# Kernel tuning notes

Hardware: AMD Instinct MI355X
Metric: run time of the kernel (lower is better)

## Reference

```python
import jax, jax.numpy as jnp
import numpy as np
from jax import lax

B, S, E, H, NB, F, NQ, NC = 256, 196, 256, 8, 4, 1024, 8, 10


def _ln(x, g, b, eps=1e-5):
    m = x.mean(-1, keepdims=True)
    v = ((x - m) ** 2).mean(-1, keepdims=True)
    return (x - m) / jnp.sqrt(v + eps) * g + b


def _pe(s, e):
    pos = jnp.arange(s, dtype=jnp.float32)[:, None]
    div = jnp.exp(jnp.arange(0, e, 2, dtype=jnp.float32) * (-np.log(10000.0) / e))
    ang = pos * div  # [S, E/2]
    # even indices sin, odd indices cos -> interleave
    return jnp.stack([jnp.sin(ang), jnp.cos(ang)], axis=-1).reshape(s, e)


def setup_inputs() -> dict:
    key = jax.random.key(0)
    ks = jax.random.split(key, 16)
    r = lambda i, shape, s=0.05: jax.random.normal(ks[i], shape, dtype=jnp.float32) * s
    return {
        'x': jax.random.normal(ks[0], (B, 4, 28, 28), dtype=jnp.float32),
        'qfilter_w': r(1, (4, 1, 2, 2), 0.3), 'qfilter_b': jnp.zeros(4, jnp.float32),
        'pw_w': r(2, (4, 4, 1, 1), 0.3), 'pw_b': jnp.zeros(4, jnp.float32),
        'embed_w': r(3, (E, 4), 0.3), 'embed_b': jnp.zeros(E, jnp.float32),
        'in_proj_w': r(4, (NB, 3 * E, E)), 'in_proj_b': jnp.zeros((NB, 3 * E), jnp.float32),
        'out_w': r(5, (NB, E, E)), 'out_b': jnp.zeros((NB, E), jnp.float32),
        'theta': r(6, (NB, NQ), 1.0),
        'l1_w': r(7, (NB, F, NQ), 0.3), 'l1_b': jnp.zeros((NB, F), jnp.float32),
        'l2_w': r(8, (NB, E, F)), 'l2_b': jnp.zeros((NB, E), jnp.float32),
        'ln1_g': jnp.ones((NB, E), jnp.float32), 'ln1_b': jnp.zeros((NB, E), jnp.float32),
        'ln2_g': jnp.ones((NB, E), jnp.float32), 'ln2_b': jnp.zeros((NB, E), jnp.float32),
        'cls_w': r(9, (NC, E)), 'cls_b': jnp.zeros(NC, jnp.float32),
    }


def reference(x, qfilter_w, qfilter_b, pw_w, pw_b, embed_w, embed_b,
              in_proj_w, in_proj_b, out_w, out_b, theta,
              l1_w, l1_b, l2_w, l2_b, ln1_g, ln1_b, ln2_g, ln2_b, cls_w, cls_b):
    dn = ('NCHW', 'OIHW', 'NCHW')
    # depthwise 2x2 stride-2 quanvolution filter (groups=4)
    feat = lax.conv_general_dilated(x, qfilter_w, (2, 2), 'VALID',
                                    dimension_numbers=dn, feature_group_count=4)
    feat = feat + qfilter_b[None, :, None, None]
    # 1x1 pointwise conv
    feat = lax.conv_general_dilated(feat, pw_w, (1, 1), 'VALID', dimension_numbers=dn)
    feat = feat + pw_b[None, :, None, None]
    b = x.shape[0]
    feat = feat.reshape(b, S, 4)  # channel-major view, faithful to torch .view
    h = feat @ embed_w.T + embed_b
    h = h + _pe(S, E)[None]
    hd = E // H
    scale = 1.0 / np.sqrt(hd)
    for i in range(NB):
        # multi-head self-attention
        qkv = h @ in_proj_w[i].T + in_proj_b[i]
        q, k, v = jnp.split(qkv, 3, axis=-1)
        q = q.reshape(b, S, H, hd).transpose(0, 2, 1, 3)
        k = k.reshape(b, S, H, hd).transpose(0, 2, 1, 3)
        v = v.reshape(b, S, H, hd).transpose(0, 2, 1, 3)
        scores = jnp.einsum('bhsd,bhtd->bhst', q, k) * scale
        a = jax.nn.softmax(scores, axis=-1)
        o = jnp.einsum('bhst,bhtd->bhsd', a, v).transpose(0, 2, 1, 3).reshape(b, S, E)
        o = o @ out_w[i].T + out_b[i]
        h = _ln(h + o, ln1_g[i], ln1_b[i])
        # quantum FFN: RX(x_j) then RY(theta_j) on |0>, <Z> = cos(x_j)cos(theta_j)
        qm = jnp.cos(h[..., :NQ]) * jnp.cos(theta[i])  # [b, S, NQ]
        f = jax.nn.relu(qm @ l1_w[i].T + l1_b[i]) @ l2_w[i].T + l2_b[i]
        h = _ln(h + f, ln2_g[i], ln2_b[i])
    pooled = h.mean(axis=1)
    return pooled @ cls_w.T + cls_b
```

## Files before the change

### kernel.cpp

```cpp
#include <hip/hip_runtime.h>
#include <math.h>

#define BATCH 256
#define SEQ   196
#define EMB   256
#define HEADS 8
#define HDIM  32
#define NBLK  4
#define FDIM  1024
#define NQB   8
#define NCLS  10
#define MROWS (BATCH*SEQ)

typedef __attribute__((ext_vector_type(8))) short  short8;
typedef __attribute__((ext_vector_type(4))) float  floatx4;

__device__ __forceinline__ unsigned short f2b(float f) {
    unsigned u = __builtin_bit_cast(unsigned, f);
    u += 0x7fffu + ((u >> 16) & 1u);
    return (unsigned short)(u >> 16);
}
__device__ __forceinline__ float b2f(unsigned short u) {
    return __builtin_bit_cast(float, ((unsigned)u) << 16);
}

__device__ __forceinline__ void gl_lds16(const void* g, void* l) {
    __builtin_amdgcn_global_load_lds(
        (const __attribute__((address_space(1))) unsigned int*)g,
        (__attribute__((address_space(3))) unsigned int*)l, 16, 0, 0);
}

#define QSCALE (0.17677669529663687f * 1.4426950408889634f)

__global__ void pe_kernel(float* __restrict__ pe) {
    int s = blockIdx.x, e = threadIdx.x;
    int j2 = (e >> 1) * 2;
    float dv  = expf(-(float)j2 * (logf(10000.0f) / (float)EMB));
    float ang = (float)s * dv;
    pe[s * EMB + e] = (e & 1) ? cosf(ang) : sinf(ang);
}

__global__ __launch_bounds__(256) void cvt_kernel(
    const float* __restrict__ src, unsigned short* __restrict__ dst, int n)
{
    int i = (blockIdx.x * 256 + threadIdx.x) * 4;
    if (i < n) {
        float4 v = *(const float4*)(src + i);
        ushort4 o;
        o.x = f2b(v.x); o.y = f2b(v.y); o.z = f2b(v.z); o.w = f2b(v.w);
        *(ushort4*)(dst + i) = o;
    }
}

__global__ __launch_bounds__(256) void l1t_kernel(
    const float* __restrict__ src, float* __restrict__ dst)
{
    int idx = blockIdx.x * 256 + threadIdx.x;
    int i = idx >> 13, rem = idx & 8191;
    int q = rem & 7, f = rem >> 3;
    dst[((size_t)i * NQB + q) * FDIM + f] = src[idx];
}

__global__ __launch_bounds__(256) void feat_kernel(
    const float* __restrict__ x,  const float* __restrict__ qw,
    const float* __restrict__ qb, const float* __restrict__ pw,
    const float* __restrict__ pb, float* __restrict__ feat)
{
    int idx = blockIdx.x * 256 + threadIdx.x;
    int bs = idx >> 2, c = idx & 3;
    int b  = bs / SEQ, s = bs % SEQ;
    int co = s / 49;
    int p  = (s % 49) * 4 + c;
    int hh = p / 14, ww = p % 14;

    float dw[4];
#pragma unroll
    for (int ci = 0; ci < 4; ++ci) {
        const float* xp = x + (((size_t)b * 4 + ci) * 28 + hh * 2) * 28 + ww * 2;
        dw[ci] = qb[ci] + xp[0]  * qw[ci * 4 + 0] + xp[1]  * qw[ci * 4 + 1]
                        + xp[28] * qw[ci * 4 + 2] + xp[29] * qw[ci * 4 + 3];
    }
    feat[idx] = pb[co] + pw[co * 4 + 0] * dw[0] + pw[co * 4 + 1] * dw[1]
                       + pw[co * 4 + 2] * dw[2] + pw[co * 4 + 3] * dw[3];
}

__global__ __launch_bounds__(256) void embed2_kernel(
    const float* __restrict__ feat, const float* __restrict__ ew,
    const float* __restrict__ eb,   const float* __restrict__ pe,
    unsigned short* __restrict__ hb)
{
    __shared__ float fL[32 * 4];
    int t = threadIdx.x;
    int base = blockIdx.x * 32;

    if (t < 128) fL[t] = feat[(size_t)base * 4 + t];
    __syncthreads();

    float4 w4  = *(const float4*)(ew + t * 4);
    float  ebv = eb[t];
    int s = base % SEQ;
#pragma unroll 4
    for (int tt = 0; tt < 32; ++tt) {
        float4 f = *(const float4*)&fL[tt * 4];
        float v = ebv + f.x * w4.x + f.y * w4.y + f.z * w4.z + f.w * w4.w
                + pe[s * EMB + t];
        hb[(size_t)(base + tt) * EMB + t] = f2b(v);
        if (++s == SEQ) s = 0;
    }
}

__global__ __launch_bounds__(512) void bgemm_kernel(
    const unsigned short* __restrict__ A, const unsigned short* __restrict__ W,
    const float* __restrict__ bias, unsigned short* __restrict__ Cb,
    int M, int N, int K, int qcols, float qscale)
{
    __shared__ unsigned short As[128 * 64];
    __shared__ unsigned short Bs[128 * 64];

    int t = threadIdx.x;
    int w = t >> 6, l = t & 63;
    int quad = l >> 4, lane16 = l & 15;
    int m0 = blockIdx.y * 128, n0 = blockIdx.x * 128;
    int mq = (w >> 2) * 64;
    int nq = (w & 3) * 32;

    int lr8  = l >> 3;
    int scol = ((l & 7) ^ lr8) * 8;
    int srow = w * 16 + lr8;
    const unsigned short* Abase = A + (size_t)(m0 + srow) * K + scol;
    const unsigned short* Wbase = W + (size_t)(n0 + srow) * K + scol;
    unsigned short* AsW = As + w * 16 * 64;
    unsigned short* BsW = Bs + w * 16 * 64;

    floatx4 acc[4][2];
#pragma unroll
    for (int i = 0; i < 4; ++i)
#pragma unroll
        for (int j = 0; j < 2; ++j) acc[i][j] = (floatx4){0.f, 0.f, 0.f, 0.f};

    int key = lane16 & 7;

    for (int k0 = 0; k0 < K; k0 += 64) {
        __syncthreads();
#pragma unroll
        for (int c = 0; c < 2; ++c) {
            gl_lds16(Abase + (size_t)c * 8 * K + k0, AsW + c * 512);
            gl_lds16(Wbase + (size_t)c * 8 * K + k0, BsW + c * 512);
        }
        __syncthreads();

#pragma unroll
        for (int kk = 0; kk < 2; ++kk) {
            int ch = ((kk * 4 + quad) ^ key) * 8;
            short8 af[4], bf[2];
#pragma unroll
            for (int i = 0; i < 4; ++i)
                af[i] = *(const short8*)&As[(mq + i * 16 + lane16) * 64 + ch];
#pragma unroll
            for (int j = 0; j < 2; ++j)
                bf[j] = *(const short8*)&Bs[(nq + j * 16 + lane16) * 64 + ch];
#pragma unroll
            for (int i = 0; i < 4; ++i)
#pragma unroll
                for (int j = 0; j < 2; ++j)
                    acc[i][j] = __builtin_amdgcn_mfma_f32_16x16x32_bf16(
                                    af[i], bf[j], acc[i][j], 0, 0, 0);
        }
    }

#pragma unroll
    for (int j = 0; j < 2; ++j) {
        int col = n0 + nq + j * 16 + lane16;
        float bb  = bias[col];
        float mul = (col < qcols) ? qscale : 1.0f;
#pragma unroll
        for (int i = 0; i < 4; ++i) {
#pragma unroll
            for (int r = 0; r < 4; ++r) {
                int row = m0 + mq + i * 16 + quad * 4 + r;
                Cb[(size_t)row * N + col] = f2b((acc[i][j][r] + bb) * mul);
            }
        }
    }
}

__global__ __launch_bounds__(512) void bgemm_ln_kernel(
    const unsigned short* __restrict__ A, const unsigned short* __restrict__ W,
    const float* __restrict__ bias, const float* __restrict__ g,
    const float* __restrict__ beta, const float* __restrict__ theta,
    const unsigned short* __restrict__ Rb, unsigned short* __restrict__ OutB,
    float* __restrict__ qm, int K)
{
    __shared__ unsigned short As[64 * 64];
    __shared__ unsigned short Bs[256 * 64];
    __shared__ float redS[64][4], redQ[64][4];
    __shared__ float mrow[64], irow[64];

    int t = threadIdx.x;
    int w = t >> 6, l = t & 63;
    int quad = l >> 4, lane16 = l & 15;
    int m0 = blockIdx.x * 64;

    int wq = w >> 2;
    int cg = w & 3;
    int nq = cg * 64;

    int lr8  = l >> 3;
    int lc8s = ((l & 7) ^ lr8) * 8;
    const unsigned short* Abase = A + (size_t)(m0 + w * 8 + lr8) * K + lc8s;
    const unsigned short* Wbase = W + (size_t)(w * 8 + lr8) * K + lc8s;
    unsigned short* AsW = As + w * 8 * 64;
    unsigned short* BsW = Bs + w * 8 * 64;

    floatx4 acc[2][4];
#pragma unroll
    for (int i = 0; i < 2; ++i)
#pragma unroll
        for (int j = 0; j < 4; ++j) acc[i][j] = (floatx4){0.f, 0.f, 0.f, 0.f};

    int key = lane16 & 7;

    for (int k0 = 0; k0 < K; k0 += 64) {
        __syncthreads();
        gl_lds16(Abase + k0, AsW);
#pragma unroll
        for (int c = 0; c < 4; ++c)
            gl_lds16(Wbase + (size_t)c * 64 * K + k0, BsW + c * 64 * 64);
        __syncthreads();

#pragma unroll
        for (int kk = 0; kk < 2; ++kk) {
            int ch = ((kk * 4 + quad) ^ key) * 8;
            short8 af[2], bf[4];
#pragma unroll
            for (int i = 0; i < 2; ++i)
                af[i] = *(const short8*)&As[(wq * 32 + i * 16 + lane16) * 64 + ch];
#pragma unroll
            for (int j = 0; j < 4; ++j)
                bf[j] = *(const short8*)&Bs[(nq + j * 16 + lane16) * 64 + ch];
#pragma unroll
            for (int i = 0; i < 2; ++i)
#pragma unroll
                for (int j = 0; j < 4; ++j)
                    acc[i][j] = __builtin_amdgcn_mfma_f32_16x16x32_bf16(
                                    af[i], bf[j], acc[i][j], 0, 0, 0);
        }
    }

    float bb[4];
#pragma unroll
    for (int j = 0; j < 4; ++j) bb[j] = bias[nq + j * 16 + lane16];

#pragma unroll
    for (int i = 0; i < 2; ++i) {
#pragma unroll
        for (int r = 0; r < 4; ++r) {
            int row = wq * 32 + i * 16 + quad * 4 + r;
            const unsigned short* rp = Rb + (size_t)(m0 + row) * EMB;
            float s1 = 0.f, s2 = 0.f;
#pragma unroll
            for (int j = 0; j < 4; ++j) {
                float v = acc[i][j][r] + bb[j] + b2f(rp[nq + j * 16 + lane16]);
                acc[i][j][r] = v;
                s1 += v;
                s2 += v * v;
            }
#pragma unroll
            for (int off = 8; off >= 1; off >>= 1) {
                s1 += __shfl_xor(s1, off);
                s2 += __shfl_xor(s2, off);
            }
            if (lane16 == 0) { redS[row][cg] = s1; redQ[row][cg] = s2; }
        }
    }
    __syncthreads();

    if (t < 64) {
        float s1 = redS[t][0] + redS[t][1] + redS[t][2] + redS[t][3];
        float s2 = redQ[t][0] + redQ[t][1] + redQ[t][2] + redQ[t][3];
        float mean = s1 * (1.0f / 256.0f);
        float var  = s2 * (1.0f / 256.0f) - mean * mean;
        mrow[t] = mean;
        irow[t] = rsqrtf(var + 1e-5f);
    }
    __syncthreads();

    float gv[4], bv[4];
#pragma unroll
    for (int j = 0; j < 4; ++j) {
        int col = nq + j * 16 + lane16;
        gv[j] = g[col];
        bv[j] = beta[col];
    }

#pragma unroll
    for (int i = 0; i < 2; ++i) {
#pragma unroll
        for (int r = 0; r < 4; ++r) {
            int row  = wq * 32 + i * 16 + quad * 4 + r;
            float mean = mrow[row], inv = irow[row];
            size_t base = (size_t)(m0 + row) * EMB;
#pragma unroll
            for (int j = 0; j < 4; ++j) {
                int col = nq + j * 16 + lane16;
                float y = (acc[i][j][r] - mean) * inv * gv[j] + bv[j];
                OutB[base + col] = f2b(y);
                if (qm && cg == 0 && j == 0 && lane16 < NQB)
                    qm[(size_t)(m0 + row) * NQB + lane16] =
                        __cosf(y) * __cosf(theta[lane16]);
            }
        }
    }
}

__global__ __launch_bounds__(256) void act_kernel(
    const float* __restrict__ qm, const float* __restrict__ l1wT,
    const float* __restrict__ l1b, unsigned short* __restrict__ act)
{
    __shared__ float qL[16 * NQB];
    int t  = threadIdx.x;
    int m0 = blockIdx.x * 16;

    if (t < 128) qL[t] = qm[(size_t)m0 * NQB + t];

    int f  = (t & 127) * 8;
    int r0 = (t >> 7) * 8;

    float4 wv0[8], wv1[8];
#pragma unroll
    for (int j = 0; j < 8; ++j) {
        wv0[j] = *(const float4*)(l1wT + (size_t)j * FDIM + f);
        wv1[j] = *(const float4*)(l1wT + (size_t)j * FDIM + f + 4);
    }
    float4 b0 = *(const float4*)(l1b + f);
    float4 b1 = *(const float4*)(l1b + f + 4);
    __syncthreads();

#pragma unroll
    for (int rr = 0; rr < 8; ++rr) {
        int row = r0 + rr;
        const float* q = &qL[row * NQB];
        float4 a0 = b0, a1 = b1;
#pragma unroll
        for (int j = 0; j < 8; ++j) {
            float qj = q[j];
            a0.x += qj * wv0[j].x; a0.y += qj * wv0[j].y;
            a0.z += qj * wv0[j].z; a0.w += qj * wv0[j].w;
            a1.x += qj * wv1[j].x; a1.y += qj * wv1[j].y;
            a1.z += qj * wv1[j].z; a1.w += qj * wv1[j].w;
        }
        unsigned short o[8];
        o[0] = f2b(fmaxf(a0.x, 0.f)); o[1] = f2b(fmaxf(a0.y, 0.f));
        o[2] = f2b(fmaxf(a0.z, 0.f)); o[3] = f2b(fmaxf(a0.w, 0.f));
        o[4] = f2b(fmaxf(a1.x, 0.f)); o[5] = f2b(fmaxf(a1.y, 0.f));
        o[6] = f2b(fmaxf(a1.z, 0.f)); o[7] = f2b(fmaxf(a1.w, 0.f));
        *(short8*)(act + (size_t)(m0 + row) * FDIM + f) = *(short8*)o;
    }
}

__global__ __launch_bounds__(256, 3) void attn_kernel(
    const unsigned short* __restrict__ qkv, unsigned short* __restrict__ ob)
{
    __shared__ unsigned short Vt[32 * 232];
    __shared__ unsigned short Ps[64 * 232];

    int t  = threadIdx.x;
    int bh = blockIdx.x;
    int b  = bh >> 3;
    int hh = bh & 7;
    const unsigned short* base = qkv + (size_t)b * SEQ * 768 + hh * HDIM;

    for (int idx = t; idx < SEQ * 8; idx += 256) {
        int s = idx >> 3, d4 = (idx & 7) * 4;
        ushort4 vv = *(const ushort4*)(base + (size_t)s * 768 + 512 + d4);
        Vt[(d4 + 0) * 232 + s] = vv.x;
        Vt[(d4 + 1) * 232 + s] = vv.y;
        Vt[(d4 + 2) * 232 + s] = vv.z;
        Vt[(d4 + 3) * 232 + s] = vv.w;
    }
    for (int idx = t; idx < 32 * 36; idx += 256) {
        int d = idx / 36, c = 196 + idx % 36;
        Vt[d * 232 + c] = 0;
    }
    for (int idx = t; idx < 64 * 24; idx += 256) {
        int r = idx / 24, c = 208 + idx % 24;
        Ps[r * 232 + c] = 0;
    }

    int w = t >> 6, l = t & 63;
    int quad = l >> 4, lane16 = l & 15;
    unsigned short* Pw = Ps + w * 16 * 232;

    short8 kf[13];
#pragma unroll
    for (int kt = 0; kt < 13; ++kt)
        kf[kt] = *(const short8*)(base + (size_t)(kt * 16 + lane16) * 768 + 256 + quad * 8);

    __syncthreads();

    for (int qt = w; qt < 13; qt += 4) {
        short8 af = *(const short8*)(base + (size_t)(qt * 16 + lane16) * 768 + quad * 8);

        floatx4 sc[13];
#pragma unroll
        for (int kt = 0; kt < 13; ++kt) {
            floatx4 z = {0.f, 0.f, 0.f, 0.f};
            sc[kt] = __builtin_amdgcn_mfma_f32_16x16x32_bf16(af, kf[kt], z, 0, 0, 0);
        }

        float lsum[4] = {0.f, 0.f, 0.f, 0.f};
#pragma unroll
        for (int kt = 0; kt < 13; ++kt) {
#pragma unroll
            for (int r = 0; r < 4; ++r) {
                float v = sc[kt][r];
                if (kt == 12 && lane16 >= 4) v = -1e30f;
                float p = exp2f(v);
                lsum[r] += p;
                Pw[(quad * 4 + r) * 232 + kt * 16 + lane16] = f2b(p);
            }
        }
#pragma unroll
        for (int off = 8; off >= 1; off >>= 1)
#pragma unroll
            for (int r = 0; r < 4; ++r)
                lsum[r] += __shfl_xor(lsum[r], off);

        floatx4 oacc[2] = {{0.f,0.f,0.f,0.f},{0.f,0.f,0.f,0.f}};
#pragma unroll
        for (int c = 0; c < 7; ++c) {
            short8 pa = *(const short8*)&Pw[lane16 * 232 + c * 32 + quad * 8];
#pragma unroll
            for (int nt = 0; nt < 2; ++nt) {
                short8 vb = *(const short8*)&Vt[(nt * 16 + lane16) * 232 + c * 32 + quad * 8];
                oacc[nt] = __builtin_amdgcn_mfma_f32_16x16x32_bf16(pa, vb, oacc[nt], 0, 0, 0);
            }
        }

#pragma unroll
        for (int r = 0; r < 4; ++r) {
            int srow = qt * 16 + quad * 4 + r;
            if (srow < SEQ) {
                float invl = 1.f / lsum[r];
                unsigned short* op = ob + ((size_t)b * SEQ + srow) * EMB + hh * HDIM;
                op[lane16]      = f2b(oacc[0][r] * invl);
                op[16 + lane16] = f2b(oacc[1][r] * invl);
            }
        }
    }
}

__global__ __launch_bounds__(256) void pool_cls_kernel(
    const unsigned short* __restrict__ hb, const float* __restrict__ cw,
    const float* __restrict__ cb, float* __restrict__ out)
{
    __shared__ float pooled[EMB];
    int b = blockIdx.x;
    int e = threadIdx.x;
    float s = 0.f;
    const unsigned short* hp = hb + (size_t)b * SEQ * EMB + e;
    for (int j = 0; j < SEQ; ++j) s += b2f(hp[(size_t)j * EMB]);
    pooled[e] = s * (1.0f / (float)SEQ);
    __syncthreads();
    if (e < NCLS) {
        float acc = cb[e];
        const float* wr = cw + e * EMB;
        for (int k = 0; k < EMB; ++k) acc += pooled[k] * wr[k];
        out[b * NCLS + e] = acc;
    }
}

extern "C" void kernel_launch(void* const* d_in, const int* in_sizes, int n_in,
                              void* d_out, int out_size, void* d_ws, size_t ws_size,
                              hipStream_t stream)
{
    const float* x         = (const float*)d_in[0];
    const float* qfilter_w = (const float*)d_in[1];
    const float* qfilter_b = (const float*)d_in[2];
    const float* pw_w      = (const float*)d_in[3];
    const float* pw_b      = (const float*)d_in[4];
    const float* embed_w   = (const float*)d_in[5];
    const float* embed_b   = (const float*)d_in[6];
    const float* in_proj_w = (const float*)d_in[7];
    const float* in_proj_b = (const float*)d_in[8];
    const float* out_w     = (const float*)d_in[9];
    const float* out_b     = (const float*)d_in[10];
    const float* theta     = (const float*)d_in[11];
    const float* l1_w      = (const float*)d_in[12];
    const float* l1_b      = (const float*)d_in[13];
    const float* l2_w      = (const float*)d_in[14];
    const float* l2_b      = (const float*)d_in[15];
    const float* ln1_g     = (const float*)d_in[16];
    const float* ln1_b     = (const float*)d_in[17];
    const float* ln2_g     = (const float*)d_in[18];
    const float* ln2_b     = (const float*)d_in[19];
    const float* cls_w     = (const float*)d_in[20];
    const float* cls_b     = (const float*)d_in[21];

    char* ws = (char*)d_ws;
    unsigned short* big = (unsigned short*)ws; ws += (size_t)MROWS * FDIM * 2;
    float* qm  = (float*)ws;                   ws += (size_t)MROWS * NQB * 4;
    float* pe  = (float*)ws;                   ws += (size_t)SEQ * EMB * 4;
    float* feat = (float*)ws;                  ws += (size_t)MROWS * 4 * 4;
    unsigned short* hb  = (unsigned short*)ws; ws += (size_t)MROWS * EMB * 2;
    unsigned short* hb1 = (unsigned short*)ws; ws += (size_t)MROWS * EMB * 2;
    unsigned short* ob  = (unsigned short*)ws; ws += (size_t)MROWS * EMB * 2;
    unsigned short* wb_in = (unsigned short*)ws; ws += (size_t)NBLK * 768 * EMB * 2;
    unsigned short* wb_o  = (unsigned short*)ws; ws += (size_t)NBLK * EMB * EMB * 2;
    unsigned short* wb_l2 = (unsigned short*)ws; ws += (size_t)NBLK * EMB * FDIM * 2;
    float* l1wT = (float*)ws;                  ws += (size_t)NBLK * NQB * FDIM * 4;

    unsigned short* qkvb = big;
    unsigned short* act  = big;

    pe_kernel<<<SEQ, EMB, 0, stream>>>(pe);
    {
        int n1 = NBLK * 768 * EMB;
        int n2 = NBLK * EMB * EMB;
        int n3 = NBLK * EMB * FDIM;
        cvt_kernel<<<n1 / 1024, 256, 0, stream>>>(in_proj_w, wb_in, n1);
        cvt_kernel<<<n2 / 1024, 256, 0, stream>>>(out_w,     wb_o,  n2);
        cvt_kernel<<<n3 / 1024, 256, 0, stream>>>(l2_w,      wb_l2, n3);
        l1t_kernel<<<(NBLK * FDIM * NQB) / 256, 256, 0, stream>>>(l1_w, l1wT);
    }

    feat_kernel<<<(MROWS * 4) / 256, 256, 0, stream>>>(
        x, qfilter_w, qfilter_b, pw_w, pw_b, feat);
    embed2_kernel<<<MROWS / 32, 256, 0, stream>>>(
        feat, embed_w, embed_b, pe, hb);

    for (int i = 0; i < NBLK; ++i) {
        bgemm_kernel<<<dim3(6, MROWS / 128), 512, 0, stream>>>(
            hb, wb_in + (size_t)i * 768 * EMB, in_proj_b + i * 768,
            qkvb, MROWS, 768, EMB, 256, QSCALE);
        attn_kernel<<<BATCH * HEADS, 256, 0, stream>>>(qkvb, ob);
        bgemm_ln_kernel<<<MROWS / 64, 512, 0, stream>>>(
            ob, wb_o + (size_t)i * EMB * EMB, out_b + i * EMB,
            ln1_g + i * EMB, ln1_b + i * EMB, theta + i * NQB,
            hb, hb1, qm, EMB);
        act_kernel<<<MROWS / 16, 256, 0, stream>>>(
            qm, l1wT + (size_t)i * NQB * FDIM, l1_b + i * FDIM, act);
        bgemm_ln_kernel<<<MROWS / 64, 512, 0, stream>>>(
            act, wb_l2 + (size_t)i * EMB * FDIM, l2_b + i * EMB,
            ln2_g + i * EMB, ln2_b + i * EMB, nullptr,
            hb1, hb, nullptr, FDIM);
    }

    pool_cls_kernel<<<BATCH, EMB, 0, stream>>>(hb, cls_w, cls_b, (float*)d_out);
}
```

Before: 939.2 us.

## Fuse FFN first layer into second GEMM+LayerNorm kernel, computing activations in LDS

Replaces the separate act_kernel and the FDIM-K bgemm_ln launch with one ffn_ln_kernel. Each 64-row tile now computes the 8-input l1 linear plus ReLU on the fly for every 64-wide K chunk and writes the result straight into shared memory as the bf16 A operand of the MFMA GEMM. This removes the write and re-read of the 50176x1024 bf16 activation buffer in global memory, and the workspace shrinks to hold only qkv. In exchange, the l1 weights are recomputed per tile, and the A-tile loading is now synchronous ALU work inside the K loop instead of an async copy.

```diff
diff --git a/kernel.cpp b/kernel.cpp
--- a/kernel.cpp
+++ b/kernel.cpp
@@ -313,48 +313,153 @@
     }
 }
 
-__global__ __launch_bounds__(256) void act_kernel(
-    const float* __restrict__ qm, const float* __restrict__ l1wT,
-    const float* __restrict__ l1b, unsigned short* __restrict__ act)
-{
-    __shared__ float qL[16 * NQB];
-    int t  = threadIdx.x;
-    int m0 = blockIdx.x * 16;
-
-    if (t < 128) qL[t] = qm[(size_t)m0 * NQB + t];
-
-    int f  = (t & 127) * 8;
-    int r0 = (t >> 7) * 8;
-
-    float4 wv0[8], wv1[8];
-#pragma unroll
-    for (int j = 0; j < 8; ++j) {
-        wv0[j] = *(const float4*)(l1wT + (size_t)j * FDIM + f);
-        wv1[j] = *(const float4*)(l1wT + (size_t)j * FDIM + f + 4);
-    }
-    float4 b0 = *(const float4*)(l1b + f);
-    float4 b1 = *(const float4*)(l1b + f + 4);
-    __syncthreads();
-
-#pragma unroll
-    for (int rr = 0; rr < 8; ++rr) {
-        int row = r0 + rr;
-        const float* q = &qL[row * NQB];
-        float4 a0 = b0, a1 = b1;
+__global__ __launch_bounds__(512) void ffn_ln_kernel(
+    const float* __restrict__ qm,  const float* __restrict__ l1wT,
+    const float* __restrict__ l1b, const unsigned short* __restrict__ W,
+    const float* __restrict__ bias, const float* __restrict__ g,
+    const float* __restrict__ beta, const unsigned short* __restrict__ Rb,
+    unsigned short* __restrict__ OutB)
+{
+    __shared__ unsigned short As[64 * 64];
+    __shared__ unsigned short Bs[256 * 64];
+    __shared__ float redS[64][4], redQ[64][4];
+    __shared__ float mrow[64], irow[64];
+
+    int t = threadIdx.x;
+    int w = t >> 6, l = t & 63;
+    int quad = l >> 4, lane16 = l & 15;
+    int m0 = blockIdx.x * 64;
+
+    int wq = w >> 2;
+    int cg = w & 3;
+    int nq = cg * 64;
+
+    int lr8  = l >> 3;
+    int lc8s = ((l & 7) ^ lr8) * 8;
+    const unsigned short* Wbase = W + (size_t)(w * 8 + lr8) * FDIM + lc8s;
+    unsigned short* BsW = Bs + w * 8 * 64;
+
+    int am = t >> 3;
+    int ag = t & 7;
+    floatx4 q0 = *(const floatx4*)(qm + (size_t)(m0 + am) * NQB);
+    floatx4 q1 = *(const floatx4*)(qm + (size_t)(m0 + am) * NQB + 4);
+    float qv[8] = {q0.x, q0.y, q0.z, q0.w, q1.x, q1.y, q1.z, q1.w};
+    unsigned short* adst = As + am * 64 + ((ag ^ (am & 7)) * 8);
+
+    floatx4 acc[2][4];
+#pragma unroll
+    for (int i = 0; i < 2; ++i)
+#pragma unroll
+        for (int j = 0; j < 4; ++j) acc[i][j] = (floatx4){0.f, 0.f, 0.f, 0.f};
+
+    int key = lane16 & 7;
+
+    for (int k0 = 0; k0 < FDIM; k0 += 64) {
+        __syncthreads();
+#pragma unroll
+        for (int c = 0; c < 4; ++c)
+            gl_lds16(Wbase + (size_t)c * 64 * FDIM + k0, BsW + c * 64 * 64);
+
+        int kb = k0 + ag * 8;
+        float4 a0 = *(const float4*)(l1b + kb);
+        float4 a1 = *(const float4*)(l1b + kb + 4);
 #pragma unroll
         for (int j = 0; j < 8; ++j) {
-            float qj = q[j];
-            a0.x += qj * wv0[j].x; a0.y += qj * wv0[j].y;
-            a0.z += qj * wv0[j].z; a0.w += qj * wv0[j].w;
-            a1.x += qj * wv1[j].x; a1.y += qj * wv1[j].y;
-            a1.z += qj * wv1[j].z; a1.w += qj * wv1[j].w;
+            float4 w0 = *(const float4*)(l1wT + (size_t)j * FDIM + kb);
+            float4 w1 = *(const float4*)(l1wT + (size_t)j * FDIM + kb + 4);
+            float qj = qv[j];
+            a0.x += qj * w0.x; a0.y += qj * w0.y;
+            a0.z += qj * w0.z; a0.w += qj * w0.w;
+            a1.x += qj * w1.x; a1.y += qj * w1.y;
+            a1.z += qj * w1.z; a1.w += qj * w1.w;
         }
         unsigned short o[8];
         o[0] = f2b(fmaxf(a0.x, 0.f)); o[1] = f2b(fmaxf(a0.y, 0.f));
         o[2] = f2b(fmaxf(a0.z, 0.f)); o[3] = f2b(fmaxf(a0.w, 0.f));
         o[4] = f2b(fmaxf(a1.x, 0.f)); o[5] = f2b(fmaxf(a1.y, 0.f));
         o[6] = f2b(fmaxf(a1.z, 0.f)); o[7] = f2b(fmaxf(a1.w, 0.f));
-        *(short8*)(act + (size_t)(m0 + row) * FDIM + f) = *(short8*)o;
+        *(short8*)adst = *(short8*)o;
+        __syncthreads();
+
+#pragma unroll
+        for (int kk = 0; kk < 2; ++kk) {
+            int ch = ((kk * 4 + quad) ^ key) * 8;
+            short8 af[2], bf[4];
+#pragma unroll
+            for (int i = 0; i < 2; ++i)
+                af[i] = *(const short8*)&As[(wq * 32 + i * 16 + lane16) * 64 + ch];
+#pragma unroll
+            for (int j = 0; j < 4; ++j)
+                bf[j] = *(const short8*)&Bs[(nq + j * 16 + lane16) * 64 + ch];
+#pragma unroll
+            for (int i = 0; i < 2; ++i)
+#pragma unroll
+                for (int j = 0; j < 4; ++j)
+                    acc[i][j] = __builtin_amdgcn_mfma_f32_16x16x32_bf16(
+                                    af[i], bf[j], acc[i][j], 0, 0, 0);
+        }
+    }
+
+    float bb[4];
+#pragma unroll
+    for (int j = 0; j < 4; ++j) bb[j] = bias[nq + j * 16 + lane16];
+
+#pragma unroll
+    for (int i = 0; i < 2; ++i) {
+#pragma unroll
+        for (int r = 0; r < 4; ++r) {
+            int row = wq * 32 + i * 16 + quad * 4 + r;
+            const unsigned short* rp = Rb + (size_t)(m0 + row) * EMB;
+            float s1 = 0.f, s2 = 0.f;
+#pragma unroll
+            for (int j = 0; j < 4; ++j) {
+                float v = acc[i][j][r] + bb[j] + b2f(rp[nq + j * 16 + lane16]);
+                acc[i][j][r] = v;
+                s1 += v;
+                s2 += v * v;
+            }
+#pragma unroll
+            for (int off = 8; off >= 1; off >>= 1) {
+                s1 += __shfl_xor(s1, off);
+                s2 += __shfl_xor(s2, off);
+            }
+            if (lane16 == 0) { redS[row][cg] = s1; redQ[row][cg] = s2; }
+        }
+    }
+    __syncthreads();
+
+    if (t < 64) {
+        float s1 = redS[t][0] + redS[t][1] + redS[t][2] + redS[t][3];
+        float s2 = redQ[t][0] + redQ[t][1] + redQ[t][2] + redQ[t][3];
+        float mean = s1 * (1.0f / 256.0f);
+        float var  = s2 * (1.0f / 256.0f) - mean * mean;
+        mrow[t] = mean;
+        irow[t] = rsqrtf(var + 1e-5f);
+    }
+    __syncthreads();
+
+    float gv[4], bv[4];
+#pragma unroll
+    for (int j = 0; j < 4; ++j) {
+        int col = nq + j * 16 + lane16;
+        gv[j] = g[col];
+        bv[j] = beta[col];
+    }
+
+#pragma unroll
+    for (int i = 0; i < 2; ++i) {
+#pragma unroll
+        for (int r = 0; r < 4; ++r) {
+            int row  = wq * 32 + i * 16 + quad * 4 + r;
+            float mean = mrow[row], inv = irow[row];
+            size_t base = (size_t)(m0 + row) * EMB;
+#pragma unroll
+            for (int j = 0; j < 4; ++j) {
+                int col = nq + j * 16 + lane16;
+                float y = (acc[i][j][r] - mean) * inv * gv[j] + bv[j];
+                OutB[base + col] = f2b(y);
+            }
+        }
     }
 }
 
@@ -498,7 +603,7 @@
     const float* cls_b     = (const float*)d_in[21];
 
     char* ws = (char*)d_ws;
-    unsigned short* big = (unsigned short*)ws; ws += (size_t)MROWS * FDIM * 2;
+    unsigned short* qkvb = (unsigned short*)ws; ws += (size_t)MROWS * 768 * 2;
     float* qm  = (float*)ws;                   ws += (size_t)MROWS * NQB * 4;
     float* pe  = (float*)ws;                   ws += (size_t)SEQ * EMB * 4;
     float* feat = (float*)ws;                  ws += (size_t)MROWS * 4 * 4;
@@ -510,9 +615,6 @@
     unsigned short* wb_l2 = (unsigned short*)ws; ws += (size_t)NBLK * EMB * FDIM * 2;
     float* l1wT = (float*)ws;                  ws += (size_t)NBLK * NQB * FDIM * 4;
 
-    unsigned short* qkvb = big;
-    unsigned short* act  = big;
-
     pe_kernel<<<SEQ, EMB, 0, stream>>>(pe);
     {
         int n1 = NBLK * 768 * EMB;
@@ -538,12 +640,10 @@
             ob, wb_o + (size_t)i * EMB * EMB, out_b + i * EMB,
             ln1_g + i * EMB, ln1_b + i * EMB, theta + i * NQB,
             hb, hb1, qm, EMB);
-        act_kernel<<<MROWS / 16, 256, 0, stream>>>(
-            qm, l1wT + (size_t)i * NQB * FDIM, l1_b + i * FDIM, act);
-        bgemm_ln_kernel<<<MROWS / 64, 512, 0, stream>>>(
-            act, wb_l2 + (size_t)i * EMB * FDIM, l2_b + i * EMB,
-            ln2_g + i * EMB, ln2_b + i * EMB, nullptr,
-            hb1, hb, nullptr, FDIM);
+        ffn_ln_kernel<<<MROWS / 64, 512, 0, stream>>>(
+            qm, l1wT + (size_t)i * NQB * FDIM, l1_b + i * FDIM,
+            wb_l2 + (size_t)i * EMB * FDIM, l2_b + i * EMB,
+            ln2_g + i * EMB, ln2_b + i * EMB, hb1, hb);
     }
 
     pool_cls_kernel<<<BATCH, EMB, 0, stream>>>(hb, cls_w, cls_b, (float*)d_out);
```

Result: slower. 1.084 ms (+15.4%).
